# Kernel optimization log

Hardware: AMD Instinct MI355X
Metric: run time of the kernel (lower is better)

## Reference

```python
import jax, jax.numpy as jnp
import numpy as np

LAMBDA_U = 0.01
MARGIN = 1.0
MAX_GROUPING_SCALE = 2.0
BETA_STATIC_THRESH = 0.15
RAND_U = 0.5  # stand-in for torch.rand(size=(1,)) scalar
COEF = jnp.ones((5,), dtype=jnp.float32)  # c_l, f_l, b_l, s_l, garfield_l


def infer_garfield(pt_encodings, weights, scales, W1, W2):
    # weighted aggregation of per-sample encodings along the ray -> [N, D]
    feat = jnp.einsum('nsd,ns->nd', pt_encodings, weights)
    x = jnp.concatenate([feat, scales[:, None]], axis=-1)  # [N, D+1]
    h = jax.nn.relu(x @ W1)
    g = h @ W2
    # unit-norm grouping feature (GARField style)
    return g / (jnp.linalg.norm(g, axis=-1, keepdims=True) + 1e-6)


def pairwise_dist(g):
    # ||g_i - g_j||_2 via gram matrix; [N, N]
    sq = jnp.sum(g * g, axis=-1)
    d2 = sq[:, None] + sq[None, :] - 2.0 * (g @ g.T)
    return jnp.sqrt(jnp.maximum(d2, 1e-12))


def setup_inputs() -> dict:
    key = jax.random.key(0)
    ks = jax.random.split(key, 12)
    N, S, D, H, F = 4096, 64, 64, 256, 256
    return {
        'rgbs': jax.random.uniform(ks[0], (N, 3), jnp.float32),
        'ray_mask': jnp.ones((N, 1), jnp.float32),
        'rgb_coarse': jax.random.uniform(ks[1], (N, 3), jnp.float32),
        'rgb_fine_combined': jax.random.uniform(ks[2], (N, 3), jnp.float32),
        'beta': jax.random.uniform(ks[3], (N,), jnp.float32),
        'transient_sigmas': jax.random.uniform(ks[4], (N, S), jnp.float32),
        'pt_encodings': jax.random.normal(ks[5], (N, S, D), jnp.float32),
        'weights_fine_static': jax.random.uniform(ks[6], (N, S), jnp.float32),
        'scales': jax.random.uniform(ks[7], (N,), jnp.float32),
        'W1': jax.random.normal(ks[8], (D + 1, H), jnp.float32) * (1.0 / np.sqrt(D + 1)),
        'W2': jax.random.normal(ks[9], (H, F), jnp.float32) * (1.0 / np.sqrt(H)),
        'sam_masks': jax.random.randint(ks[10], (N,), 0, 64, jnp.int64),
        'chunk_size': 256,
    }


def reference(rgbs, ray_mask, rgb_coarse, rgb_fine_combined, beta, transient_sigmas,
              pt_encodings, weights_fine_static, scales, W1, W2, sam_masks, chunk_size):
    msum = ray_mask.sum() + 1e-20
    c_l = 0.5 * (((rgb_coarse - rgbs) ** 2) * ray_mask).sum() / msum
    f_l = (((rgb_fine_combined - rgbs) ** 2) / (2.0 * beta[:, None] ** 2) * ray_mask).sum() / msum
    b_l = 3.0 + (jnp.log(beta) * ray_mask[:, 0]).sum() / msum
    s_l = LAMBDA_U * transient_sigmas.mean()

    N = sam_masks.shape[0]
    labels1 = sam_masks[:, None]
    labels2 = sam_masks[None, :]
    mask_pos = labels1 == labels2
    mask_neg = ~mask_pos

    idx = jnp.arange(N)
    # kron(eye(num_chunks), ones(chunk,chunk)) then triu(diagonal=0)
    same_chunk = (idx[:, None] // chunk_size) == (idx[None, :] // chunk_size)
    block_mask = same_chunk & (idx[None, :] >= idx[:, None])
    block_mask = block_mask & (labels1 != -1) & (labels2 != -1)
    diag = idx[:, None] == idx[None, :]
    static = beta < BETA_STATIC_THRESH
    static_mask = static[:, None] | static[None, :]

    pos_mask = mask_pos & block_mask & (~diag) & static_mask
    neg_mask = mask_neg & block_mask & static_mask

    g = infer_garfield(pt_encodings, weights_fine_static, scales, W1, W2)
    d = pairwise_dist(g)
    loss1 = jnp.where(pos_mask, d, 0.0).sum()

    scale_diff = jnp.maximum(0.0, MAX_GROUPING_SCALE - scales)
    larger_scale = scales + scale_diff * RAND_U
    g_ls = infer_garfield(pt_encodings, weights_fine_static, larger_scale, W1, W2)
    d_ls = pairwise_dist(g_ls)
    loss2 = jnp.where(pos_mask, d_ls, 0.0).sum()

    loss4 = jnp.where(neg_mask, jax.nn.relu(MARGIN - d), 0.0).sum()

    garfield_l = (loss1 + loss2 + loss4) / block_mask.sum()

    return jnp.stack([c_l, f_l, b_l, s_l, garfield_l]) * COEF
```

## Files before the change

### kernel.cpp

```cpp
#include <hip/hip_runtime.h>
#include <math.h>

#define NN 4096
#define SS 64
#define DD 64
#define HH 256
#define FF 256

__device__ __forceinline__ float waveReduce(float v) {
#pragma unroll
  for (int o = 32; o > 0; o >>= 1) v += __shfl_down(v, o, 64);
  return v;
}

__global__ void k_zero(double* __restrict__ acc) {
  if (threadIdx.x < 16) acc[threadIdx.x] = 0.0;
}

__global__ void k_scalar(const float* __restrict__ rgbs, const float* __restrict__ ray_mask,
                         const float* __restrict__ coarse, const float* __restrict__ fine,
                         const float* __restrict__ beta, const float* __restrict__ sig,
                         double* __restrict__ acc) {
  int tid = blockIdx.x * blockDim.x + threadIdx.x;
  float c = 0.f, f = 0.f, b = 0.f, m = 0.f, s = 0.f;
  if (tid < NN) {
    float mk = ray_mask[tid];
    float bt = beta[tid];
    float inv2b2 = 1.0f / (2.0f * bt * bt);
#pragma unroll
    for (int ch = 0; ch < 3; ++ch) {
      float r = rgbs[tid * 3 + ch];
      float dc = coarse[tid * 3 + ch] - r;
      float df = fine[tid * 3 + ch] - r;
      c += dc * dc * mk;
      f += df * df * inv2b2 * mk;
    }
    c *= 0.5f;
    b = logf(bt) * mk;
    m = mk;
  }
  for (int i = tid; i < NN * SS; i += NN) s += sig[i];
  c = waveReduce(c); f = waveReduce(f); b = waveReduce(b); m = waveReduce(m); s = waveReduce(s);
  if ((threadIdx.x & 63) == 0) {
    atomicAdd(&acc[0], (double)c);
    atomicAdd(&acc[1], (double)f);
    atomicAdd(&acc[2], (double)b);
    atomicAdd(&acc[3], (double)m);
    atomicAdd(&acc[4], (double)s);
  }
}

__global__ void k_feat(const float* __restrict__ pt, const float* __restrict__ w,
                       float* __restrict__ feat) {
  int wave = (blockIdx.x * blockDim.x + threadIdx.x) >> 6;
  int lane = threadIdx.x & 63;
  if (wave >= NN) return;
  const float4* p4 = (const float4*)(pt + (size_t)wave * SS * DD);
  const float* wr = w + wave * SS;
  float a0 = 0.f, a1 = 0.f, a2 = 0.f, a3 = 0.f;
#pragma unroll
  for (int it = 0; it < 16; ++it) {
    float4 v = p4[it * 64 + lane];
    float ws = wr[it * 4 + (lane >> 4)];
    a0 += v.x * ws; a1 += v.y * ws; a2 += v.z * ws; a3 += v.w * ws;
  }
  a0 += __shfl_xor(a0, 16, 64); a1 += __shfl_xor(a1, 16, 64);
  a2 += __shfl_xor(a2, 16, 64); a3 += __shfl_xor(a3, 16, 64);
  a0 += __shfl_xor(a0, 32, 64); a1 += __shfl_xor(a1, 32, 64);
  a2 += __shfl_xor(a2, 32, 64); a3 += __shfl_xor(a3, 32, 64);
  if (lane < 16) {
    float4 o = make_float4(a0, a1, a2, a3);
    ((float4*)(feat + wave * DD))[lane] = o;
  }
}

__global__ void k_h(const float* __restrict__ feat, const float* __restrict__ scales,
                    const float* __restrict__ W1, float* __restrict__ h, int larger) {
  int j = threadIdx.x;
  int n0 = blockIdx.x * 4;
  __shared__ float sf[4][DD];
  __shared__ float ss[4];
  if (j < 64) ((float4*)sf)[j] = ((const float4*)(feat + n0 * DD))[j];
  if (j < 4) {
    float sc = scales[n0 + j];
    if (larger) sc = sc + fmaxf(0.f, 2.0f - sc) * 0.5f;
    ss[j] = sc;
  }
  __syncthreads();
  float a0 = 0.f, a1 = 0.f, a2 = 0.f, a3 = 0.f;
#pragma unroll 4
  for (int k = 0; k < DD; k += 4) {
    float w0 = W1[(k + 0) * HH + j];
    float w1 = W1[(k + 1) * HH + j];
    float w2 = W1[(k + 2) * HH + j];
    float w3 = W1[(k + 3) * HH + j];
    float4 s0 = *(const float4*)&sf[0][k];
    float4 s1 = *(const float4*)&sf[1][k];
    float4 s2 = *(const float4*)&sf[2][k];
    float4 s3 = *(const float4*)&sf[3][k];
    a0 += s0.x * w0 + s0.y * w1 + s0.z * w2 + s0.w * w3;
    a1 += s1.x * w0 + s1.y * w1 + s1.z * w2 + s1.w * w3;
    a2 += s2.x * w0 + s2.y * w1 + s2.z * w2 + s2.w * w3;
    a3 += s3.x * w0 + s3.y * w1 + s3.z * w2 + s3.w * w3;
  }
  float wl = W1[64 * HH + j];
  a0 += ss[0] * wl; a1 += ss[1] * wl; a2 += ss[2] * wl; a3 += ss[3] * wl;
  h[(n0 + 0) * HH + j] = fmaxf(a0, 0.f);
  h[(n0 + 1) * HH + j] = fmaxf(a1, 0.f);
  h[(n0 + 2) * HH + j] = fmaxf(a2, 0.f);
  h[(n0 + 3) * HH + j] = fmaxf(a3, 0.f);
}

__global__ void k_g(const float* __restrict__ h, const float* __restrict__ W2,
                    float* __restrict__ g, float* __restrict__ gT, float* __restrict__ sqn) {
  int f = threadIdx.x;
  int n0 = blockIdx.x * 8;
  __shared__ float sh[8][HH];
  __shared__ float ssq[8];
#pragma unroll
  for (int it = 0; it < 2; ++it)
    ((float4*)sh)[it * 256 + f] = ((const float4*)(h + n0 * HH))[it * 256 + f];
  if (f < 8) ssq[f] = 0.f;
  __syncthreads();
  float a[8];
#pragma unroll
  for (int r = 0; r < 8; ++r) a[r] = 0.f;
  for (int k = 0; k < HH; k += 4) {
    float w0 = W2[(k + 0) * FF + f];
    float w1 = W2[(k + 1) * FF + f];
    float w2 = W2[(k + 2) * FF + f];
    float w3 = W2[(k + 3) * FF + f];
#pragma unroll
    for (int r = 0; r < 8; ++r) {
      float4 s4 = *(const float4*)&sh[r][k];
      a[r] += s4.x * w0 + s4.y * w1 + s4.z * w2 + s4.w * w3;
    }
  }
#pragma unroll
  for (int r = 0; r < 8; ++r) {
    float s = waveReduce(a[r] * a[r]);
    if ((threadIdx.x & 63) == 0) atomicAdd(&ssq[r], s);
  }
  __syncthreads();
#pragma unroll
  for (int r = 0; r < 8; ++r) {
    float inv = 1.0f / (sqrtf(ssq[r]) + 1e-6f);
    a[r] *= inv;
    g[(n0 + r) * FF + f] = a[r];
  }
  if (f < 8) {
    float inv = 1.0f / (sqrtf(ssq[f]) + 1e-6f);
    sqn[n0 + f] = ssq[f] * inv * inv;
  }
  float4 v0 = make_float4(a[0], a[1], a[2], a[3]);
  float4 v1 = make_float4(a[4], a[5], a[6], a[7]);
  float4* dst = (float4*)(gT + (size_t)f * NN + n0);
  dst[0] = v0; dst[1] = v1;
}

__global__ void k_pair(const float* __restrict__ g, const float* __restrict__ gT,
                       const float* __restrict__ sqn, const int* __restrict__ labels,
                       const float* __restrict__ beta, double* __restrict__ acc, int pass) {
  int c = blockIdx.x >> 5;
  int ig = blockIdx.x & 31;
  int t = threadIdx.x >> 6;
  int lane = threadIdx.x & 63;
  int i0 = c * 256 + ig * 8;
  __shared__ float sgi[8][FF];
  __shared__ float ssqi[8];
  __shared__ int sli[8];
  __shared__ int sst[8];
#pragma unroll
  for (int it = 0; it < 2; ++it)
    ((float4*)sgi)[it * 256 + threadIdx.x] = ((const float4*)(g + (size_t)i0 * FF))[it * 256 + threadIdx.x];
  if (threadIdx.x < 8) {
    int i = i0 + threadIdx.x;
    ssqi[threadIdx.x] = sqn[i];
    sli[threadIdx.x] = labels[i];
    sst[threadIdx.x] = beta[i] < 0.15f ? 1 : 0;
  }
  __syncthreads();

  float fl1 = 0.f, fl4 = 0.f, fcnt = 0.f;
  if (t * 64 + 63 >= ig * 8) {
    int jl = t * 64 + lane;
    int jg = c * 256 + jl;
    const float* gtc = gT + jg;
    float accum[8];
#pragma unroll
    for (int r = 0; r < 8; ++r) accum[r] = 0.f;
    for (int k = 0; k < FF; k += 4) {
      float v0 = gtc[(size_t)(k + 0) * NN];
      float v1 = gtc[(size_t)(k + 1) * NN];
      float v2 = gtc[(size_t)(k + 2) * NN];
      float v3 = gtc[(size_t)(k + 3) * NN];
#pragma unroll
      for (int r = 0; r < 8; ++r) {
        float4 s4 = *(const float4*)&sgi[r][k];
        accum[r] += s4.x * v0 + s4.y * v1 + s4.z * v2 + s4.w * v3;
      }
    }
    int lj = labels[jg];
    float sqj = sqn[jg];
    int statj = beta[jg] < 0.15f ? 1 : 0;
#pragma unroll
    for (int r = 0; r < 8; ++r) {
      int il = ig * 8 + r;
      if (jl >= il) {
        int li = sli[r];
        if (li != -1 && lj != -1) {
          fcnt += 1.0f;
          int stat = sst[r] | statj;
          if (stat) {
            float d2 = ssqi[r] + sqj - 2.0f * accum[r];
            float d = sqrtf(fmaxf(d2, 1e-12f));
            if (li == lj) {
              if (jl != il) fl1 += d;
            } else {
              fl4 += fmaxf(0.f, 1.0f - d);
            }
          }
        }
      }
    }
  }
  fl1 = waveReduce(fl1);
  fl4 = waveReduce(fl4);
  fcnt = waveReduce(fcnt);
  if (lane == 0) {
    if (pass == 0) {
      atomicAdd(&acc[5], (double)fl1);
      atomicAdd(&acc[7], (double)fl4);
      atomicAdd(&acc[8], (double)fcnt);
    } else {
      atomicAdd(&acc[6], (double)fl1);
    }
  }
}

__global__ void k_final(const double* __restrict__ acc, float* __restrict__ out) {
  if (threadIdx.x == 0) {
    double msum = acc[3] + 1e-20;
    out[0] = (float)(acc[0] / msum);
    out[1] = (float)(acc[1] / msum);
    out[2] = (float)(3.0 + acc[2] / msum);
    out[3] = (float)(0.01 * acc[4] / (double)(NN * SS));
    out[4] = (float)((acc[5] + acc[6] + acc[7]) / acc[8]);
  }
}

extern "C" void kernel_launch(void* const* d_in, const int* in_sizes, int n_in,
                              void* d_out, int out_size, void* d_ws, size_t ws_size,
                              hipStream_t stream) {
  const float* rgbs      = (const float*)d_in[0];
  const float* ray_mask  = (const float*)d_in[1];
  const float* rgb_coarse= (const float*)d_in[2];
  const float* rgb_fine  = (const float*)d_in[3];
  const float* beta      = (const float*)d_in[4];
  const float* sig       = (const float*)d_in[5];
  const float* pt        = (const float*)d_in[6];
  const float* wfs       = (const float*)d_in[7];
  const float* scales    = (const float*)d_in[8];
  const float* W1        = (const float*)d_in[9];
  const float* W2        = (const float*)d_in[10];
  const int*   labels    = (const int*)d_in[11];
  float* out = (float*)d_out;

  char* w = (char*)d_ws;
  double* acc = (double*)w;
  float* feat = (float*)(w + 256);
  float* h    = feat + NN * DD;
  float* g    = h + NN * HH;
  float* gT   = g + NN * FF;
  float* sqn  = gT + NN * FF;

  k_zero<<<1, 64, 0, stream>>>(acc);
  k_scalar<<<16, 256, 0, stream>>>(rgbs, ray_mask, rgb_coarse, rgb_fine, beta, sig, acc);
  k_feat<<<1024, 256, 0, stream>>>(pt, wfs, feat);

  k_h<<<1024, 256, 0, stream>>>(feat, scales, W1, h, 0);
  k_g<<<512, 256, 0, stream>>>(h, W2, g, gT, sqn);
  k_pair<<<512, 256, 0, stream>>>(g, gT, sqn, labels, beta, acc, 0);

  k_h<<<1024, 256, 0, stream>>>(feat, scales, W1, h, 1);
  k_g<<<512, 256, 0, stream>>>(h, W2, g, gT, sqn);
  k_pair<<<512, 256, 0, stream>>>(g, gT, sqn, labels, beta, acc, 1);

  k_final<<<1, 64, 0, stream>>>(acc, out);
}
```

Before: 328.6 us.

## Register-tile MLP and pairwise GEMMs with float4 outputs and split-K wave reduction

Rewrites k_h, k_g and k_pair so each thread computes a 4-wide column tile using float4 weight and gT loads. The per-row operands now come straight from global memory instead of being staged in shared memory. k_g and k_pair split the K dimension across waves or lane groups and reduce partials through shared memory or xor shuffles. Atomics are skipped when a partial sum is zero. This aims to raise arithmetic per load and cut the number of blocks, at the cost of more redundant global reads of the row vectors and extra reduction work.

```diff
diff --git a/kernel.cpp b/kernel.cpp
--- a/kernel.cpp
+++ b/kernel.cpp
@@ -10,6 +10,11 @@
 __device__ __forceinline__ float waveReduce(float v) {
 #pragma unroll
   for (int o = 32; o > 0; o >>= 1) v += __shfl_down(v, o, 64);
+  return v;
+}
+__device__ __forceinline__ float waveReduceXor(float v) {
+#pragma unroll
+  for (int o = 32; o > 0; o >>= 1) v += __shfl_xor(v, o, 64);
   return v;
 }
 
@@ -76,148 +81,161 @@
 
 __global__ void k_h(const float* __restrict__ feat, const float* __restrict__ scales,
                     const float* __restrict__ W1, float* __restrict__ h, int larger) {
-  int j = threadIdx.x;
-  int n0 = blockIdx.x * 4;
-  __shared__ float sf[4][DD];
-  __shared__ float ss[4];
-  if (j < 64) ((float4*)sf)[j] = ((const float4*)(feat + n0 * DD))[j];
-  if (j < 4) {
-    float sc = scales[n0 + j];
+  int w = threadIdx.x >> 6, lane = threadIdx.x & 63;
+  int j0 = 4 * lane;
+  int nb = blockIdx.x * 16 + w * 4;
+  float a[4][4];
+#pragma unroll
+  for (int r = 0; r < 4; ++r)
+#pragma unroll
+    for (int jj = 0; jj < 4; ++jj) a[r][jj] = 0.f;
+#pragma unroll 8
+  for (int k = 0; k < DD; ++k) {
+    float4 wv = *(const float4*)&W1[k * HH + j0];
+#pragma unroll
+    for (int r = 0; r < 4; ++r) {
+      float fv = feat[(nb + r) * DD + k];
+      a[r][0] += fv * wv.x; a[r][1] += fv * wv.y;
+      a[r][2] += fv * wv.z; a[r][3] += fv * wv.w;
+    }
+  }
+  float4 wl = *(const float4*)&W1[DD * HH + j0];
+#pragma unroll
+  for (int r = 0; r < 4; ++r) {
+    float sc = scales[nb + r];
     if (larger) sc = sc + fmaxf(0.f, 2.0f - sc) * 0.5f;
-    ss[j] = sc;
-  }
-  __syncthreads();
-  float a0 = 0.f, a1 = 0.f, a2 = 0.f, a3 = 0.f;
-#pragma unroll 4
-  for (int k = 0; k < DD; k += 4) {
-    float w0 = W1[(k + 0) * HH + j];
-    float w1 = W1[(k + 1) * HH + j];
-    float w2 = W1[(k + 2) * HH + j];
-    float w3 = W1[(k + 3) * HH + j];
-    float4 s0 = *(const float4*)&sf[0][k];
-    float4 s1 = *(const float4*)&sf[1][k];
-    float4 s2 = *(const float4*)&sf[2][k];
-    float4 s3 = *(const float4*)&sf[3][k];
-    a0 += s0.x * w0 + s0.y * w1 + s0.z * w2 + s0.w * w3;
-    a1 += s1.x * w0 + s1.y * w1 + s1.z * w2 + s1.w * w3;
-    a2 += s2.x * w0 + s2.y * w1 + s2.z * w2 + s2.w * w3;
-    a3 += s3.x * w0 + s3.y * w1 + s3.z * w2 + s3.w * w3;
-  }
-  float wl = W1[64 * HH + j];
-  a0 += ss[0] * wl; a1 += ss[1] * wl; a2 += ss[2] * wl; a3 += ss[3] * wl;
-  h[(n0 + 0) * HH + j] = fmaxf(a0, 0.f);
-  h[(n0 + 1) * HH + j] = fmaxf(a1, 0.f);
-  h[(n0 + 2) * HH + j] = fmaxf(a2, 0.f);
-  h[(n0 + 3) * HH + j] = fmaxf(a3, 0.f);
+    float4 o;
+    o.x = fmaxf(a[r][0] + sc * wl.x, 0.f);
+    o.y = fmaxf(a[r][1] + sc * wl.y, 0.f);
+    o.z = fmaxf(a[r][2] + sc * wl.z, 0.f);
+    o.w = fmaxf(a[r][3] + sc * wl.w, 0.f);
+    *(float4*)&h[(nb + r) * HH + j0] = o;
+  }
 }
 
 __global__ void k_g(const float* __restrict__ h, const float* __restrict__ W2,
                     float* __restrict__ g, float* __restrict__ gT, float* __restrict__ sqn) {
-  int f = threadIdx.x;
   int n0 = blockIdx.x * 8;
-  __shared__ float sh[8][HH];
-  __shared__ float ssq[8];
-#pragma unroll
-  for (int it = 0; it < 2; ++it)
-    ((float4*)sh)[it * 256 + f] = ((const float4*)(h + n0 * HH))[it * 256 + f];
-  if (f < 8) ssq[f] = 0.f;
+  int w = threadIdx.x >> 6, lane = threadIdx.x & 63;
+  int j0 = 4 * lane;
+  int kb = w * 64;
+  float a[8][4];
+#pragma unroll
+  for (int r = 0; r < 8; ++r)
+#pragma unroll
+    for (int jj = 0; jj < 4; ++jj) a[r][jj] = 0.f;
+#pragma unroll 8
+  for (int kk = 0; kk < 64; kk += 4) {
+    int k = kb + kk;
+    float4 w0 = *(const float4*)&W2[(k + 0) * FF + j0];
+    float4 w1 = *(const float4*)&W2[(k + 1) * FF + j0];
+    float4 w2 = *(const float4*)&W2[(k + 2) * FF + j0];
+    float4 w3 = *(const float4*)&W2[(k + 3) * FF + j0];
+#pragma unroll
+    for (int r = 0; r < 8; ++r) {
+      float4 hv = *(const float4*)&h[(n0 + r) * HH + k];
+      a[r][0] += hv.x * w0.x + hv.y * w1.x + hv.z * w2.x + hv.w * w3.x;
+      a[r][1] += hv.x * w0.y + hv.y * w1.y + hv.z * w2.y + hv.w * w3.y;
+      a[r][2] += hv.x * w0.z + hv.y * w1.z + hv.z * w2.z + hv.w * w3.z;
+      a[r][3] += hv.x * w0.w + hv.y * w1.w + hv.z * w2.w + hv.w * w3.w;
+    }
+  }
+  __shared__ float red[4][64][33];
+  __shared__ float trans[8][FF];
+#pragma unroll
+  for (int r = 0; r < 8; ++r)
+#pragma unroll
+    for (int jj = 0; jj < 4; ++jj) red[w][lane][4 * r + jj] = a[r][jj];
   __syncthreads();
-  float a[8];
-#pragma unroll
-  for (int r = 0; r < 8; ++r) a[r] = 0.f;
-  for (int k = 0; k < HH; k += 4) {
-    float w0 = W2[(k + 0) * FF + f];
-    float w1 = W2[(k + 1) * FF + f];
-    float w2 = W2[(k + 2) * FF + f];
-    float w3 = W2[(k + 3) * FF + f];
-#pragma unroll
-    for (int r = 0; r < 8; ++r) {
-      float4 s4 = *(const float4*)&sh[r][k];
-      a[r] += s4.x * w0 + s4.y * w1 + s4.z * w2 + s4.w * w3;
-    }
-  }
-#pragma unroll
-  for (int r = 0; r < 8; ++r) {
-    float s = waveReduce(a[r] * a[r]);
-    if ((threadIdx.x & 63) == 0) atomicAdd(&ssq[r], s);
+#pragma unroll
+  for (int rr = 0; rr < 2; ++rr) {
+    int r = 2 * w + rr;
+    float d0 = red[0][lane][4 * r + 0] + red[1][lane][4 * r + 0] + red[2][lane][4 * r + 0] + red[3][lane][4 * r + 0];
+    float d1 = red[0][lane][4 * r + 1] + red[1][lane][4 * r + 1] + red[2][lane][4 * r + 1] + red[3][lane][4 * r + 1];
+    float d2 = red[0][lane][4 * r + 2] + red[1][lane][4 * r + 2] + red[2][lane][4 * r + 2] + red[3][lane][4 * r + 2];
+    float d3 = red[0][lane][4 * r + 3] + red[1][lane][4 * r + 3] + red[2][lane][4 * r + 3] + red[3][lane][4 * r + 3];
+    float ss = waveReduceXor(d0 * d0 + d1 * d1 + d2 * d2 + d3 * d3);
+    float inv = 1.0f / (sqrtf(ss) + 1e-6f);
+    float4 v = make_float4(d0 * inv, d1 * inv, d2 * inv, d3 * inv);
+    *(float4*)&g[(size_t)(n0 + r) * FF + j0] = v;
+    if (lane == 0) sqn[n0 + r] = ss * inv * inv;
+    ((float4*)&trans[r][0])[lane] = v;
   }
   __syncthreads();
-#pragma unroll
-  for (int r = 0; r < 8; ++r) {
-    float inv = 1.0f / (sqrtf(ssq[r]) + 1e-6f);
-    a[r] *= inv;
-    g[(n0 + r) * FF + f] = a[r];
-  }
-  if (f < 8) {
-    float inv = 1.0f / (sqrtf(ssq[f]) + 1e-6f);
-    sqn[n0 + f] = ssq[f] * inv * inv;
-  }
-  float4 v0 = make_float4(a[0], a[1], a[2], a[3]);
-  float4 v1 = make_float4(a[4], a[5], a[6], a[7]);
-  float4* dst = (float4*)(gT + (size_t)f * NN + n0);
-  dst[0] = v0; dst[1] = v1;
+  int tj = threadIdx.x;
+  float4 lo = make_float4(trans[0][tj], trans[1][tj], trans[2][tj], trans[3][tj]);
+  float4 hi = make_float4(trans[4][tj], trans[5][tj], trans[6][tj], trans[7][tj]);
+  *(float4*)(gT + (size_t)tj * NN + n0) = lo;
+  *(float4*)(gT + (size_t)tj * NN + n0 + 4) = hi;
 }
 
 __global__ void k_pair(const float* __restrict__ g, const float* __restrict__ gT,
                        const float* __restrict__ sqn, const int* __restrict__ labels,
                        const float* __restrict__ beta, double* __restrict__ acc, int pass) {
-  int c = blockIdx.x >> 5;
-  int ig = blockIdx.x & 31;
-  int t = threadIdx.x >> 6;
+  int c = blockIdx.x >> 5, ig = blockIdx.x & 31;
+  int i0 = c * 256 + ig * 8;
+  int wv = threadIdx.x >> 6;
   int lane = threadIdx.x & 63;
-  int i0 = c * 256 + ig * 8;
-  __shared__ float sgi[8][FF];
-  __shared__ float ssqi[8];
-  __shared__ int sli[8];
-  __shared__ int sst[8];
-#pragma unroll
-  for (int it = 0; it < 2; ++it)
-    ((float4*)sgi)[it * 256 + threadIdx.x] = ((const float4*)(g + (size_t)i0 * FF))[it * 256 + threadIdx.x];
-  if (threadIdx.x < 8) {
-    int i = i0 + threadIdx.x;
-    ssqi[threadIdx.x] = sqn[i];
-    sli[threadIdx.x] = labels[i];
-    sst[threadIdx.x] = beta[i] < 0.15f ? 1 : 0;
-  }
-  __syncthreads();
-
+  int ksub = lane >> 4;
+  int jl0 = wv * 64 + (lane & 15) * 4;
   float fl1 = 0.f, fl4 = 0.f, fcnt = 0.f;
-  if (t * 64 + 63 >= ig * 8) {
-    int jl = t * 64 + lane;
-    int jg = c * 256 + jl;
-    const float* gtc = gT + jg;
-    float accum[8];
-#pragma unroll
-    for (int r = 0; r < 8; ++r) accum[r] = 0.f;
-    for (int k = 0; k < FF; k += 4) {
-      float v0 = gtc[(size_t)(k + 0) * NN];
-      float v1 = gtc[(size_t)(k + 1) * NN];
-      float v2 = gtc[(size_t)(k + 2) * NN];
-      float v3 = gtc[(size_t)(k + 3) * NN];
+  if (wv * 64 + 63 >= ig * 8) {
+    float a[8][4];
+#pragma unroll
+    for (int r = 0; r < 8; ++r)
+#pragma unroll
+      for (int jj = 0; jj < 4; ++jj) a[r][jj] = 0.f;
+    int kb = ksub * 64;
+    const float* gtb = gT + (size_t)c * 256 + jl0;
+#pragma unroll 8
+    for (int kk = 0; kk < 64; kk += 4) {
+      int k = kb + kk;
+      float4 b0 = *(const float4*)(gtb + (size_t)(k + 0) * NN);
+      float4 b1 = *(const float4*)(gtb + (size_t)(k + 1) * NN);
+      float4 b2 = *(const float4*)(gtb + (size_t)(k + 2) * NN);
+      float4 b3 = *(const float4*)(gtb + (size_t)(k + 3) * NN);
 #pragma unroll
       for (int r = 0; r < 8; ++r) {
-        float4 s4 = *(const float4*)&sgi[r][k];
-        accum[r] += s4.x * v0 + s4.y * v1 + s4.z * v2 + s4.w * v3;
+        float4 gi = *(const float4*)(g + (size_t)(i0 + r) * FF + k);
+        a[r][0] += gi.x * b0.x + gi.y * b1.x + gi.z * b2.x + gi.w * b3.x;
+        a[r][1] += gi.x * b0.y + gi.y * b1.y + gi.z * b2.y + gi.w * b3.y;
+        a[r][2] += gi.x * b0.z + gi.y * b1.z + gi.z * b2.z + gi.w * b3.z;
+        a[r][3] += gi.x * b0.w + gi.y * b1.w + gi.z * b2.w + gi.w * b3.w;
       }
     }
-    int lj = labels[jg];
-    float sqj = sqn[jg];
-    int statj = beta[jg] < 0.15f ? 1 : 0;
-#pragma unroll
-    for (int r = 0; r < 8; ++r) {
-      int il = ig * 8 + r;
-      if (jl >= il) {
-        int li = sli[r];
-        if (li != -1 && lj != -1) {
-          fcnt += 1.0f;
-          int stat = sst[r] | statj;
-          if (stat) {
-            float d2 = ssqi[r] + sqj - 2.0f * accum[r];
-            float d = sqrtf(fmaxf(d2, 1e-12f));
-            if (li == lj) {
-              if (jl != il) fl1 += d;
-            } else {
-              fl4 += fmaxf(0.f, 1.0f - d);
+#pragma unroll
+    for (int r = 0; r < 8; ++r)
+#pragma unroll
+      for (int jj = 0; jj < 4; ++jj) {
+        float v = a[r][jj];
+        v += __shfl_xor(v, 16, 64);
+        v += __shfl_xor(v, 32, 64);
+        a[r][jj] = v;
+      }
+    if (ksub == 0) {
+#pragma unroll
+      for (int r = 0; r < 8; ++r) {
+        int i = i0 + r, il = ig * 8 + r;
+        int li = labels[i];
+        float sqi = sqn[i];
+        bool sti = beta[i] < 0.15f;
+#pragma unroll
+        for (int jj = 0; jj < 4; ++jj) {
+          int jl = jl0 + jj;
+          if (jl >= il) {
+            int jg = c * 256 + jl;
+            int lj = labels[jg];
+            if (li != -1 && lj != -1) {
+              fcnt += 1.0f;
+              if (sti || beta[jg] < 0.15f) {
+                float d2 = sqi + sqn[jg] - 2.0f * a[r][jj];
+                float d = sqrtf(fmaxf(d2, 1e-12f));
+                if (li == lj) {
+                  if (jl != il) fl1 += d;
+                } else {
+                  fl4 += fmaxf(0.f, 1.0f - d);
+                }
+              }
             }
           }
         }
@@ -229,11 +247,11 @@
   fcnt = waveReduce(fcnt);
   if (lane == 0) {
     if (pass == 0) {
-      atomicAdd(&acc[5], (double)fl1);
-      atomicAdd(&acc[7], (double)fl4);
-      atomicAdd(&acc[8], (double)fcnt);
+      if (fl1 != 0.f) atomicAdd(&acc[5], (double)fl1);
+      if (fl4 != 0.f) atomicAdd(&acc[7], (double)fl4);
+      if (fcnt != 0.f) atomicAdd(&acc[8], (double)fcnt);
     } else {
-      atomicAdd(&acc[6], (double)fl1);
+      if (fl1 != 0.f) atomicAdd(&acc[6], (double)fl1);
     }
   }
 }
@@ -278,11 +296,11 @@
   k_scalar<<<16, 256, 0, stream>>>(rgbs, ray_mask, rgb_coarse, rgb_fine, beta, sig, acc);
   k_feat<<<1024, 256, 0, stream>>>(pt, wfs, feat);
 
-  k_h<<<1024, 256, 0, stream>>>(feat, scales, W1, h, 0);
+  k_h<<<256, 256, 0, stream>>>(feat, scales, W1, h, 0);
   k_g<<<512, 256, 0, stream>>>(h, W2, g, gT, sqn);
   k_pair<<<512, 256, 0, stream>>>(g, gT, sqn, labels, beta, acc, 0);
 
-  k_h<<<1024, 256, 0, stream>>>(feat, scales, W1, h, 1);
+  k_h<<<256, 256, 0, stream>>>(feat, scales, W1, h, 1);
   k_g<<<512, 256, 0, stream>>>(h, W2, g, gT, sqn);
   k_pair<<<512, 256, 0, stream>>>(g, gT, sqn, labels, beta, acc, 1);
 
```

Result: slower. 393.1 us (+19.6%).
